# Performance work log

Hardware: AMD Instinct MI355X
Metric: run time of the kernel (lower is better)

Reference implementation:

```python
import math
import jax, jax.numpy as jnp
import numpy as np

B, S, D, H = 4, 2048, 1024, 16
DK = D // H
TINY = 1e-13  # tiny_value_of_dtype(float32) in the original masked_fill


def setup_inputs() -> dict:
    key = jax.random.key(0)
    ks = jax.random.split(key, 12)
    scale = 1.0 / math.sqrt(D)
    inp = {
        "query": jax.random.normal(ks[0], (B, S, D), jnp.float32),
        "key": jax.random.normal(ks[1], (B, S, D), jnp.float32),
        "value": jax.random.normal(ks[2], (B, S, D), jnp.float32),
        "mask": jax.random.randint(ks[3], (B, S, S), 0, 2, jnp.int32),
        "Wq": jax.random.normal(ks[4], (D, D), jnp.float32) * scale,
        "bq": jnp.zeros((D,), jnp.float32),
        "Wk": jax.random.normal(ks[5], (D, D), jnp.float32) * scale,
        "bk": jnp.zeros((D,), jnp.float32),
        "Wv": jax.random.normal(ks[6], (D, D), jnp.float32) * scale,
        "bv": jnp.zeros((D,), jnp.float32),
        "Wo": jax.random.normal(ks[7], (D, D), jnp.float32) * scale,
        "bo": jnp.zeros((D,), jnp.float32),
    }
    return inp


def _split_heads(x):
    # [B, S, D] -> [B, H, S, DK]
    return x.reshape(B, -1, H, DK).transpose(0, 2, 1, 3)


def reference(query, key, value, mask, Wq, bq, Wk, bk, Wv, bv, Wo, bo):
    q = _split_heads(query @ Wq.T + bq)
    k = _split_heads(key @ Wk.T + bk)
    v = _split_heads(value @ Wv.T + bv)
    # scores: [B, H, Sq, Sk]
    scores = jnp.einsum("bhqd,bhkd->bhqk", q, k) / math.sqrt(DK)
    # non-standard mask fill: replace masked positions with TINY (not -inf)
    m = mask[:, None, :, :] == 0  # [B,1,Sq,Sk] broadcast over heads
    scores = jnp.where(m, jnp.float32(TINY), scores)
    p_attn = jax.nn.softmax(scores, axis=-1)
    # dropout is identity in eval/reference mode
    x = jnp.einsum("bhqk,bhkd->bhqd", p_attn, v)
    x = x.transpose(0, 2, 1, 3).reshape(B, -1, D)
    return x @ Wo.T + bo
```

## Files before the change

### kernel.cpp

```cpp
#include <hip/hip_runtime.h>


typedef __attribute__((ext_vector_type(8))) short bf16x8;
typedef __attribute__((ext_vector_type(4))) float f32x4;
typedef __attribute__((ext_vector_type(16))) float f32x16;
typedef __attribute__((ext_vector_type(4))) unsigned short us4;
typedef unsigned long long u64;
typedef unsigned short u16;
typedef unsigned int u32;

#define DEV static __device__ __forceinline__

DEV u16 f2bf(float f) {
  union { float f; unsigned u; } v; v.f = f;
  return (u16)((v.u + 0x7fffu + ((v.u >> 16) & 1u)) >> 16);
}

DEV u32 cvtpk(float lo, float hi) {
  u32 r;
  asm("v_cvt_pk_bf16_f32 %0, %1, %2" : "=v"(r) : "v"(lo), "v"(hi));
  return r;
}

DEV void plswap(u32& x, u32& y) {
  asm("v_permlane32_swap_b32 %0, %1" : "+v"(x), "+v"(y));
}

DEV float fexp2(float x) {
#if __has_builtin(__builtin_amdgcn_exp2f)
  return __builtin_amdgcn_exp2f(x);
#else
  float r;
  asm volatile("v_exp_f32 %0, %1\n\ts_nop 1" : "=v"(r) : "v"(x));
  return r;
#endif
}

DEV int sbfe1(u32 w, int pos) {
#if __has_builtin(__builtin_amdgcn_sbfe)
  return __builtin_amdgcn_sbfe((int)w, pos, 1);
#else
  return ((int)(w << (31 - pos))) >> 31;
#endif
}

DEV float fmask(float s, int m) {
  union { float f; int i; } u; u.f = s; u.i &= m; return u.f;
}

DEV void gl16(const u16* g, u16* l) {
  __builtin_amdgcn_global_load_lds(
      (const __attribute__((address_space(1))) unsigned int*)g,
      (__attribute__((address_space(3))) unsigned int*)l, 16, 0, 0);
}

DEV int swz(int row, int slot) { return slot ^ (row & 7); }

__global__ void prep_kernel(const float4* __restrict__ q, const float4* __restrict__ k,
                            const float4* __restrict__ v, const float4* __restrict__ wq,
                            const float4* __restrict__ wk, const float4* __restrict__ wv,
                            const float4* __restrict__ wo, const int* __restrict__ mask,
                            us4* __restrict__ xq, us4* __restrict__ xk, us4* __restrict__ xv,
                            us4* __restrict__ owq, us4* __restrict__ owk,
                            us4* __restrict__ owv, us4* __restrict__ owo,
                            u64* __restrict__ bits) {
  const int bid = blockIdx.x;
  if (bid < 28672) {
    const float4* src; us4* dst; int base;
    if (bid < 8192)       { src = q;  dst = xq;  base = 0; }
    else if (bid < 16384) { src = k;  dst = xk;  base = 8192; }
    else if (bid < 24576) { src = v;  dst = xv;  base = 16384; }
    else if (bid < 25600) { src = wq; dst = owq; base = 24576; }
    else if (bid < 26624) { src = wk; dst = owk; base = 25600; }
    else if (bid < 27648) { src = wv; dst = owv; base = 26624; }
    else                  { src = wo; dst = owo; base = 27648; }
    const int i = (bid - base) * 256 + threadIdx.x;
    const float4 t = src[i];
    us4 r = {f2bf(t.x), f2bf(t.y), f2bf(t.z), f2bf(t.w)};
    dst[i] = r;
  } else {
    const int i = (bid - 28672) * 256 + threadIdx.x;
    const u64 bm = __ballot(mask[i] != 0);
    if ((threadIdx.x & 63) == 0) bits[i >> 6] = bm;
  }
}

template <int MODE>
DEV void gemm_body(const u16* __restrict__ P, const u16* __restrict__ Q,
                   const float* __restrict__ bias, void* __restrict__ outp,
                   int pr0, int qr0, u16* lsP, u16* lsQ) {
  constexpr int K = 1024;
  const int tid = threadIdx.x;
  const int w = tid >> 6, lane = tid & 63;
  const int wm = w >> 1, wn = w & 1;
  const int lo = lane & 15, hi = lane >> 4;
  const int srow = lane >> 3, sslot = lane & 7;

  f32x4 acc[4][4];
#pragma unroll
  for (int i = 0; i < 4; ++i)
#pragma unroll
    for (int j = 0; j < 4; ++j) acc[i][j] = (f32x4){0.f, 0.f, 0.f, 0.f};

  for (int kt = 0; kt < K; kt += 64) {
#pragma unroll
    for (int j = 0; j < 4; ++j) {
      const int c = w * 4 + j;
      const int row = c * 8 + srow;
      const int gs = swz(row, sslot);
      gl16(P + (pr0 + row) * K + kt + gs * 8, &lsP[c * 512]);
      gl16(Q + (qr0 + row) * K + kt + gs * 8, &lsQ[c * 512]);
    }
    __syncthreads();
#pragma unroll
    for (int kk = 0; kk < 2; ++kk) {
      bf16x8 af[4], bfr[4];
#pragma unroll
      for (int mf = 0; mf < 4; ++mf) {
        const int r = wm * 64 + mf * 16 + lo;
        af[mf] = *(const bf16x8*)&lsP[r * 64 + swz(r, kk * 4 + hi) * 8];
      }
#pragma unroll
      for (int nf = 0; nf < 4; ++nf) {
        const int r = wn * 64 + nf * 16 + lo;
        bfr[nf] = *(const bf16x8*)&lsQ[r * 64 + swz(r, kk * 4 + hi) * 8];
      }
#pragma unroll
      for (int mf = 0; mf < 4; ++mf)
#pragma unroll
        for (int nf = 0; nf < 4; ++nf)
          acc[mf][nf] = __builtin_amdgcn_mfma_f32_16x16x32_bf16(af[mf], bfr[nf], acc[mf][nf], 0, 0, 0);
    }
    __syncthreads();
  }

#pragma unroll
  for (int mf = 0; mf < 4; ++mf) {
#pragma unroll
    for (int nf = 0; nf < 4; ++nf) {
#pragma unroll
      for (int i = 0; i < 4; ++i) {
        const int gm = pr0 + wm * 64 + mf * 16 + hi * 4 + i;
        const int gn = qr0 + wn * 64 + nf * 16 + lo;
        float val = acc[mf][nf][i];
        if constexpr (MODE == 0 || MODE == 3) {
          val += bias[gn];
          if constexpr (MODE == 3) val *= 0.18033688011112042f;
          const int b = gm >> 11, s = gm & 2047, h = gn >> 6, dk = gn & 63;
          ((u16*)outp)[(((b * 16 + h) * 2048 + s) * 64) + dk] = f2bf(val);
        } else if constexpr (MODE == 1) {
          val += bias[gm];
          const int h = gm >> 6, dk = gm & 63, b = gn >> 11, s = gn & 2047;
          ((u16*)outp)[(((b * 16 + h) * 64 + dk) * 2048) + s] = f2bf(val);
        } else {
          val += bias[gn];
          ((float*)outp)[(size_t)gm * 1024 + gn] = val;
        }
      }
    }
  }
}

__launch_bounds__(256)
__global__ void gemm_qkv(const u16* __restrict__ xq, const u16* __restrict__ xk,
                         const u16* __restrict__ xv, const u16* __restrict__ wq,
                         const u16* __restrict__ wk, const u16* __restrict__ wv,
                         const float* __restrict__ bq, const float* __restrict__ bk,
                         const float* __restrict__ bv, u16* __restrict__ q16,
                         u16* __restrict__ k16, u16* __restrict__ vt16) {
  __shared__ u16 lsP[128 * 64];
  __shared__ u16 lsQ[128 * 64];
  const int z = blockIdx.z;
  if (z == 0)      gemm_body<3>(xq, wq, bq, q16,  blockIdx.x * 128, blockIdx.y * 128, lsP, lsQ);
  else if (z == 1) gemm_body<0>(xk, wk, bk, k16,  blockIdx.x * 128, blockIdx.y * 128, lsP, lsQ);
  else             gemm_body<1>(wv, xv, bv, vt16, blockIdx.y * 128, blockIdx.x * 128, lsP, lsQ);
}

__launch_bounds__(256)
__global__ void gemm_out(const u16* __restrict__ P, const u16* __restrict__ Q,
                         const float* __restrict__ bias, float* __restrict__ outp) {
  __shared__ u16 lsP[128 * 64];
  __shared__ u16 lsQ[128 * 64];
  gemm_body<2>(P, Q, bias, outp, blockIdx.x * 128, blockIdx.y * 128, lsP, lsQ);
}

__launch_bounds__(256, 4)
__global__ void attn_kernel(const u16* __restrict__ q16, const u16* __restrict__ k16,
                            const u16* __restrict__ vt16, const u64* __restrict__ mb,
                            u16* __restrict__ x16) {
  __shared__ u16 lsK[2][64 * 64];
  __shared__ u16 lsV[2][64 * 64];
  const int bh = blockIdx.x;
  const int b = bh >> 4, h = bh & 15;
  const int w = threadIdx.x >> 6, lane = threadIdx.x & 63;
  const int l5 = lane & 31, h1 = lane >> 5, l7 = l5 & 7;
  const int h4 = h1 * 4;
  const int q0 = blockIdx.y * 128 + w * 32;
  const u16* qbase = q16 + (size_t)bh * 2048 * 64;
  const u16* kbase = k16 + (size_t)bh * 2048 * 64;
  const u16* vbase = vt16 + (size_t)bh * 64 * 2048;
  const u64* mrow = mb + ((size_t)b * 2048 + q0 + l5) * 32;

  const int srow = lane >> 3, sslot = lane & 7;
  const int c0 = w * 2;

  const f32x16 z16 = (f32x16)(0.f);

  bf16x8 qf[4];
#pragma unroll
  for (int step = 0; step < 4; ++step)
    qf[step] = *(const bf16x8*)&qbase[(q0 + l5) * 64 + step * 16 + h1 * 8];

  f32x16 acc[2];
  acc[0] = z16; acc[1] = z16;
  float lp0 = 0.f, lp1 = 0.f, lp2 = 0.f, lp3 = 0.f;

#pragma unroll
  for (int j = 0; j < 2; ++j) {
    const int c = c0 + j, row = c * 8 + srow;
    const int gs = swz(row, sslot) * 8;
    gl16(kbase + row * 64 + gs, &lsK[0][c * 512]);
    gl16(vbase + row * 2048 + gs, &lsV[0][c * 512]);
  }

  for (int t = 0; t < 32; ++t) {
    const int cur = t & 1;
    __syncthreads();

    if (t < 31) {
      const int kv1 = (t + 1) * 64;
#pragma unroll
      for (int j = 0; j < 2; ++j) {
        const int c = c0 + j, row = c * 8 + srow;
        const int gs = swz(row, sslot) * 8;
        gl16(kbase + (kv1 + row) * 64 + gs, &lsK[cur ^ 1][c * 512]);
        gl16(vbase + row * 2048 + kv1 + gs, &lsV[cur ^ 1][c * 512]);
      }
    }

    const u64 mw = mrow[t];

    f32x16 s[2];
    __builtin_amdgcn_s_setprio(1);
#pragma unroll
    for (int f = 0; f < 2; ++f) {
      f32x16 sv = z16;
#pragma unroll
      for (int step = 0; step < 4; ++step) {
        const int row = f * 32 + l5;
        const bf16x8 kf = *(const bf16x8*)&lsK[cur][row * 64 + ((step * 2 + h1) ^ l7) * 8];
        sv = __builtin_amdgcn_mfma_f32_32x32x16_bf16(kf, qf[step], sv, 0, 0, 0);
      }
      s[f] = sv;
    }
    __builtin_amdgcn_s_setprio(0);

#pragma unroll
    for (int f = 0; f < 2; ++f) {
      const u32 wf = ((f == 0) ? (u32)mw : (u32)(mw >> 32)) >> h4;
      float p[16];
#pragma unroll
      for (int r = 0; r < 16; ++r) {
        const int pos = (r & 3) + 8 * (r >> 2);
        const int m = sbfe1(wf, pos);
        p[r] = fexp2(fmask(s[f][r], m));
      }
      lp0 += (p[0] + p[4]) + (p[8] + p[12]);
      lp1 += (p[1] + p[5]) + (p[9] + p[13]);
      lp2 += (p[2] + p[6]) + (p[10] + p[14]);
      lp3 += (p[3] + p[7]) + (p[11] + p[15]);
      u32 pk[8];
#pragma unroll
      for (int i = 0; i < 4; ++i) {
        pk[2 * i]     = cvtpk(p[4 * i],     p[4 * i + 1]);
        pk[2 * i + 1] = cvtpk(p[4 * i + 2], p[4 * i + 3]);
      }
      plswap(pk[0], pk[2]); plswap(pk[1], pk[3]);
      plswap(pk[4], pk[6]); plswap(pk[5], pk[7]);

#pragma unroll
      for (int mm = 0; mm < 2; ++mm) {
        const int m = f * 2 + mm;
        union { u32 u[4]; bf16x8 v; } pu;
        pu.u[0] = pk[4 * mm]; pu.u[1] = pk[4 * mm + 1];
        pu.u[2] = pk[4 * mm + 2]; pu.u[3] = pk[4 * mm + 3];
        __builtin_amdgcn_s_setprio(1);
#pragma unroll
        for (int db = 0; db < 2; ++db) {
          const int row = db * 32 + l5;
          const bf16x8 vf = *(const bf16x8*)&lsV[cur][row * 64 + ((m * 2 + h1) ^ l7) * 8];
          acc[db] = __builtin_amdgcn_mfma_f32_32x32x16_bf16(vf, pu.v, acc[db], 0, 0, 0);
        }
        __builtin_amdgcn_s_setprio(0);
      }
    }
  }

  const float lpart = (lp0 + lp1) + (lp2 + lp3);
  const float tot = lpart + __shfl_xor(lpart, 32, 64);
  const float inv = 1.0f / tot;

  u16* orow = x16 + ((size_t)b * 2048 + q0 + l5) * 1024 + h * 64;
#pragma unroll
  for (int db = 0; db < 2; ++db)
#pragma unroll
    for (int r = 0; r < 16; r += 2) {
      const int d = db * 32 + (r & 3) + 8 * (r >> 2) + h4;
      *(u32*)&orow[d] = cvtpk(acc[db][r] * inv, acc[db][r + 1] * inv);
    }
}

extern "C" void kernel_launch(void* const* d_in, const int* in_sizes, int n_in,
                              void* d_out, int out_size, void* d_ws, size_t ws_size,
                              hipStream_t stream) {
  const float* query = (const float*)d_in[0];
  const float* key   = (const float*)d_in[1];
  const float* value = (const float*)d_in[2];
  const int*   mask  = (const int*)d_in[3];
  const float* Wq = (const float*)d_in[4];
  const float* bq = (const float*)d_in[5];
  const float* Wk = (const float*)d_in[6];
  const float* bk = (const float*)d_in[7];
  const float* Wv = (const float*)d_in[8];
  const float* bv = (const float*)d_in[9];
  const float* Wo = (const float*)d_in[10];
  const float* bo = (const float*)d_in[11];

  char* ws = (char*)d_ws;
  const size_t MB = 1024 * 1024;
  u16* xq   = (u16*)(ws + 0);
  u16* xk   = (u16*)(ws + 16 * MB);
  u16* xv   = (u16*)(ws + 32 * MB);
  u16* wq16 = (u16*)(ws + 48 * MB);
  u16* wk16 = (u16*)(ws + 50 * MB);
  u16* wv16 = (u16*)(ws + 52 * MB);
  u16* wo16 = (u16*)(ws + 54 * MB);
  u16* q16  = (u16*)(ws + 56 * MB);
  u16* k16  = (u16*)(ws + 72 * MB);
  u16* vt16 = (u16*)(ws + 88 * MB);
  u64* mbits = (u64*)(ws + 104 * MB);
  u16* x16  = xq;

  prep_kernel<<<94208, 256, 0, stream>>>(
      (const float4*)query, (const float4*)key, (const float4*)value,
      (const float4*)Wq, (const float4*)Wk, (const float4*)Wv, (const float4*)Wo,
      mask, (us4*)xq, (us4*)xk, (us4*)xv,
      (us4*)wq16, (us4*)wk16, (us4*)wv16, (us4*)wo16, mbits);

  gemm_qkv<<<dim3(64, 8, 3), 256, 0, stream>>>(xq, xk, xv, wq16, wk16, wv16,
                                               bq, bk, bv, q16, k16, vt16);

  attn_kernel<<<dim3(64, 16), 256, 0, stream>>>(q16, k16, vt16, mbits, x16);

  gemm_out<<<dim3(64, 8), 256, 0, stream>>>(x16, wo16, bo, (float*)d_out);
}
```

Baseline: 238.7 us.

## Split attention over two KV halves with a separate combine kernel

```diff
diff --git a/kernel.cpp b/kernel.cpp
--- a/kernel.cpp
+++ b/kernel.cpp
@@ -14,6 +14,10 @@
 DEV u16 f2bf(float f) {
   union { float f; unsigned u; } v; v.f = f;
   return (u16)((v.u + 0x7fffu + ((v.u >> 16) & 1u)) >> 16);
+}
+
+DEV float bf2f(u16 x) {
+  union { float f; u32 u; } v; v.u = (u32)x << 16; return v.f;
 }
 
 DEV u32 cvtpk(float lo, float hi) {
@@ -187,23 +191,24 @@
 __launch_bounds__(256, 4)
 __global__ void attn_kernel(const u16* __restrict__ q16, const u16* __restrict__ k16,
                             const u16* __restrict__ vt16, const u64* __restrict__ mb,
-                            u16* __restrict__ x16) {
+                            u16* __restrict__ oout, float* __restrict__ lsums) {
   __shared__ u16 lsK[2][64 * 64];
-  __shared__ u16 lsV[2][64 * 64];
+  __shared__ u16 lsV[64 * 64];
   const int bh = blockIdx.x;
-  const int b = bh >> 4, h = bh & 15;
+  const int b = bh >> 4;
+  const int half = blockIdx.z;
   const int w = threadIdx.x >> 6, lane = threadIdx.x & 63;
   const int l5 = lane & 31, h1 = lane >> 5, l7 = l5 & 7;
   const int h4 = h1 * 4;
   const int q0 = blockIdx.y * 128 + w * 32;
+  const int kvbase = half * 1024;
   const u16* qbase = q16 + (size_t)bh * 2048 * 64;
   const u16* kbase = k16 + (size_t)bh * 2048 * 64;
   const u16* vbase = vt16 + (size_t)bh * 64 * 2048;
-  const u64* mrow = mb + ((size_t)b * 2048 + q0 + l5) * 32;
+  const u64* mrow = mb + ((size_t)b * 2048 + q0 + l5) * 32 + half * 16;
 
   const int srow = lane >> 3, sslot = lane & 7;
   const int c0 = w * 2;
-
   const f32x16 z16 = (f32x16)(0.f);
 
   bf16x8 qf[4];
@@ -219,22 +224,26 @@
   for (int j = 0; j < 2; ++j) {
     const int c = c0 + j, row = c * 8 + srow;
     const int gs = swz(row, sslot) * 8;
-    gl16(kbase + row * 64 + gs, &lsK[0][c * 512]);
-    gl16(vbase + row * 2048 + gs, &lsV[0][c * 512]);
-  }
-
-  for (int t = 0; t < 32; ++t) {
+    gl16(kbase + (kvbase + row) * 64 + gs, &lsK[0][c * 512]);
+  }
+
+  for (int t = 0; t < 16; ++t) {
     const int cur = t & 1;
+    const int kv0 = kvbase + t * 64;
     __syncthreads();
 
-    if (t < 31) {
-      const int kv1 = (t + 1) * 64;
+#pragma unroll
+    for (int j = 0; j < 2; ++j) {
+      const int c = c0 + j, row = c * 8 + srow;
+      const int gs = swz(row, sslot) * 8;
+      gl16(vbase + row * 2048 + kv0 + gs, &lsV[c * 512]);
+    }
+    if (t < 15) {
 #pragma unroll
       for (int j = 0; j < 2; ++j) {
         const int c = c0 + j, row = c * 8 + srow;
         const int gs = swz(row, sslot) * 8;
-        gl16(kbase + (kv1 + row) * 64 + gs, &lsK[cur ^ 1][c * 512]);
-        gl16(vbase + row * 2048 + kv1 + gs, &lsV[cur ^ 1][c * 512]);
+        gl16(kbase + (kv0 + 64 + row) * 64 + gs, &lsK[cur ^ 1][c * 512]);
       }
     }
 
@@ -277,6 +286,8 @@
       }
       plswap(pk[0], pk[2]); plswap(pk[1], pk[3]);
       plswap(pk[4], pk[6]); plswap(pk[5], pk[7]);
+
+      if (f == 0) __syncthreads();
 
 #pragma unroll
       for (int mm = 0; mm < 2; ++mm) {
@@ -288,7 +299,7 @@
 #pragma unroll
         for (int db = 0; db < 2; ++db) {
           const int row = db * 32 + l5;
-          const bf16x8 vf = *(const bf16x8*)&lsV[cur][row * 64 + ((m * 2 + h1) ^ l7) * 8];
+          const bf16x8 vf = *(const bf16x8*)&lsV[row * 64 + ((m * 2 + h1) ^ l7) * 8];
           acc[db] = __builtin_amdgcn_mfma_f32_32x32x16_bf16(vf, pu.v, acc[db], 0, 0, 0);
         }
         __builtin_amdgcn_s_setprio(0);
@@ -298,16 +309,35 @@
 
   const float lpart = (lp0 + lp1) + (lp2 + lp3);
   const float tot = lpart + __shfl_xor(lpart, 32, 64);
-  const float inv = 1.0f / tot;
-
-  u16* orow = x16 + ((size_t)b * 2048 + q0 + l5) * 1024 + h * 64;
+  const int bhq = bh * 2048 + q0 + l5;
+  if (h1 == 0) lsums[half * 131072 + bhq] = tot;
+
+  u16* orow = oout + ((size_t)half * 131072 + bhq) * 64;
 #pragma unroll
   for (int db = 0; db < 2; ++db)
 #pragma unroll
     for (int r = 0; r < 16; r += 2) {
       const int d = db * 32 + (r & 3) + 8 * (r >> 2) + h4;
-      *(u32*)&orow[d] = cvtpk(acc[db][r] * inv, acc[db][r + 1] * inv);
-    }
+      *(u32*)&orow[d] = cvtpk(acc[db][r], acc[db][r + 1]);
+    }
+}
+
+__global__ void combine_kernel(const u16* __restrict__ o, const float* __restrict__ ls,
+                               u16* __restrict__ x16) {
+  const int i = blockIdx.x * 256 + threadIdx.x;
+  const int bhq = i >> 3, d0 = (i & 7) << 3;
+  const float inv = 1.0f / (ls[bhq] + ls[bhq + 131072]);
+  const bf16x8 a = *(const bf16x8*)&o[(size_t)bhq * 64 + d0];
+  const bf16x8 c = *(const bf16x8*)&o[(size_t)bhq * 64 + d0 + 8388608];
+  const int bh = bhq >> 11, q = bhq & 2047, b = bh >> 4, h = bh & 15;
+  u32 out[4];
+#pragma unroll
+  for (int j = 0; j < 4; ++j) {
+    const float f0 = (bf2f((u16)a[2 * j])     + bf2f((u16)c[2 * j]))     * inv;
+    const float f1 = (bf2f((u16)a[2 * j + 1]) + bf2f((u16)c[2 * j + 1])) * inv;
+    out[j] = cvtpk(f0, f1);
+  }
+  *(uint4*)&x16[((size_t)b * 2048 + q) * 1024 + h * 64 + d0] = *(const uint4*)out;
 }
 
 extern "C" void kernel_launch(void* const* d_in, const int* in_sizes, int n_in,
@@ -339,7 +369,9 @@
   u16* k16  = (u16*)(ws + 72 * MB);
   u16* vt16 = (u16*)(ws + 88 * MB);
   u64* mbits = (u64*)(ws + 104 * MB);
-  u16* x16  = xq;
+  u16*  ohalf = xq;
+  u16*  x16c  = xv;
+  float* lsums = (float*)wq16;
 
   prep_kernel<<<94208, 256, 0, stream>>>(
       (const float4*)query, (const float4*)key, (const float4*)value,
@@ -350,7 +382,10 @@
   gemm_qkv<<<dim3(64, 8, 3), 256, 0, stream>>>(xq, xk, xv, wq16, wk16, wv16,
                                                bq, bk, bv, q16, k16, vt16);
 
-  attn_kernel<<<dim3(64, 16), 256, 0, stream>>>(q16, k16, vt16, mbits, x16);
-
-  gemm_out<<<dim3(64, 8), 256, 0, stream>>>(x16, wo16, bo, (float*)d_out);
-}
+  attn_kernel<<<dim3(64, 16, 2), 256, 0, stream>>>(q16, k16, vt16, mbits,
+                                                   ohalf, lsums);
+
+  combine_kernel<<<4096, 256, 0, stream>>>(ohalf, lsums, x16c);
+
+  gemm_out<<<dim3(64, 8), 256, 0, stream>>>(x16c, wo16, bo, (float*)d_out);
+}
```

Result: slower. 248.8 us (+4.2%).
